# Optimization experiments

Measured on AMD Instinct MI355X. Metric: run time of the kernel, lower is better.

Reference implementation:

```python
import jax, jax.numpy as jnp
import numpy as np

NEG_SLOPE = 0.01  # torch nn.LeakyReLU default
N_NODES, N_EDGES, N_BATCH, L_PATH = 100000, 300000, 50000, 4
D_EMB, D_HID, N_HEADS = 128, 64, 8


def setup_inputs() -> dict:
    key = jax.random.key(0)
    ks = jax.random.split(key, 10)
    return {
        "batch_nodes": jax.random.randint(ks[0], (N_BATCH,), 0, N_NODES),
        "metapath_indices": jax.random.randint(ks[1], (N_EDGES, L_PATH), 0, N_NODES),
        "edge_dst": jax.random.randint(ks[2], (N_EDGES,), 0, N_NODES),
        "transformed_feature": jax.random.normal(ks[3], (N_NODES, D_EMB), jnp.float32),
        "W_i": jax.random.normal(ks[4], (D_HID, D_EMB), jnp.float32) * 0.05,
        "W_p": jax.random.normal(ks[5], (D_HID, D_EMB), jnp.float32) * 0.05,
        "attn": jax.random.normal(ks[6], (1, N_HEADS, D_HID), jnp.float32) * 0.05,
        "W_th": jax.random.normal(ks[7], (N_HEADS, N_HEADS), jnp.float32) * 0.3,
        "W_gate": jax.random.normal(ks[8], (1, D_HID), jnp.float32) * 0.1,
        "b_gate": jnp.zeros((1,), jnp.float32),
    }


def reference(batch_nodes, metapath_indices, edge_dst, transformed_feature,
              W_i, W_p, attn, W_th, W_gate, b_gate):
    N = transformed_feature.shape[0]
    # node_type_specific_agg for mtype==1: h_src/h_dst through linear_i, h_p1/h_p2 through linear_p
    membd = transformed_feature[metapath_indices]                      # [E, 4, D_emb]
    edata = (membd[:, 0] + membd[:, 3]) @ W_i.T \
          + (membd[:, 1] + membd[:, 2]) @ W_p.T                        # [E, D]
    E, D = edata.shape
    H = attn.shape[1]
    # cat([edata]*H, dim=1).view(-1, H, D) duplicates edata per head
    efeat = jnp.broadcast_to(edata[:, None, :], (E, H, D))             # [E, H, D]
    # talking-heads attention logits, leaky-relu
    logits = (efeat * attn).sum(-1) @ W_th.T                           # [E, H]
    logits = jax.nn.leaky_relu(logits, NEG_SLOPE)
    # dgl edge_softmax: per-dst-node, per-head softmax over incoming edges (stable)
    m = jax.ops.segment_max(logits, edge_dst, num_segments=N)          # [N, H]
    ex = jnp.exp(logits - m[edge_dst])                                 # [E, H]
    den = jax.ops.segment_sum(ex, edge_dst, num_segments=N)            # [N, H]
    a = ex / den[edge_dst]                                             # [E, H]  (dropout rate 0)
    # message passing: ft = efeature * a, summed per dst node
    msgs = (efeat * a[:, :, None]).reshape(E, H * D)
    node_ft = jax.ops.segment_sum(msgs, edge_dst, num_segments=N)      # [N, H*D]
    result = node_ft[batch_nodes].reshape(-1, H, D)                    # [B, H, D]
    # gated multi-head attention: gate = mean over batch of fc_gate(result)
    gate = jnp.mean(result @ W_gate.T + b_gate, axis=0)                # [H, 1]
    result = result * gate[None]                                       # [B, H, D]
    return result.reshape(-1, H * D)
```

## Files before the change

### kernel.cpp

```cpp
#include <hip/hip_runtime.h>
#include <cstdint>
#include <cstddef>


typedef __attribute__((ext_vector_type(8))) short bf16x8;
typedef __attribute__((ext_vector_type(4))) float f32x4;

__device__ __forceinline__ unsigned short f2bf(float f) {
    unsigned u = __float_as_uint(f);
    unsigned r = u + 0x7fffu + ((u >> 16) & 1u);
    return (unsigned short)(r >> 16);
}
__device__ __forceinline__ float bf2f(unsigned short h) {
    return __uint_as_float((unsigned)h << 16);
}

__global__ __launch_bounds__(256) void k_prep(
    const float* __restrict__ Wi, const float* __restrict__ Wp,
    unsigned short* __restrict__ Whi, unsigned short* __restrict__ Wlo,
    const int* __restrict__ batch_nodes, int* __restrict__ mult, int B) {
    int t = blockIdx.x * 256 + threadIdx.x;
    if (t < B) atomicAdd(&mult[batch_nodes[t]], 1);
    if (t >= 16384) return;
    int j = t & 7, L = (t >> 3) & 63, c = (t >> 9) & 7, s = t >> 12;
    int k = s * 32 + (L >> 4) * 8 + j;
    int n = c * 16 + (L & 15);
    float v = (n < 64) ? Wi[n * 128 + k] : Wp[(n - 64) * 128 + k];
    unsigned short h = f2bf(v);
    Whi[t] = h;
    Wlo[t] = f2bf(v - bf2f(h));
}

__global__ __launch_bounds__(256) void k_dense(
    const float* __restrict__ feat, const unsigned short* __restrict__ Whi,
    const unsigned short* __restrict__ Wlo, const float* __restrict__ attn,
    unsigned short* __restrict__ Ybf, float* __restrict__ P, int M) {
    __shared__ unsigned short sBh[4096];
    __shared__ unsigned short sBl[4096];
    int t = threadIdx.x;
    int wave = t >> 6;
    int L = t & 63;
    int m = L & 15, q = L >> 4;
    int R0 = blockIdx.x * 64 + wave * 16;

    f32x4 acc[8];
#pragma unroll
    for (int c = 0; c < 8; ++c) acc[c] = (f32x4){0.f, 0.f, 0.f, 0.f};

    int rowc = R0 + m; if (rowc > M - 1) rowc = M - 1;
    const float* arow = feat + (size_t)rowc * 128;

    for (int s = 0; s < 4; ++s) {
        __syncthreads();
        {
            bf16x8* shp = (bf16x8*)sBh;
            bf16x8* slp = (bf16x8*)sBl;
            const bf16x8* gh = (const bf16x8*)(Whi + s * 4096);
            const bf16x8* gl = (const bf16x8*)(Wlo + s * 4096);
            shp[t] = gh[t]; shp[t + 256] = gh[t + 256];
            slp[t] = gl[t]; slp[t + 256] = gl[t + 256];
        }
        __syncthreads();

        const float4* ap = (const float4*)(arow + s * 32 + q * 8);
        float4 a0 = ap[0], a1 = ap[1];
        float av[8] = {a0.x, a0.y, a0.z, a0.w, a1.x, a1.y, a1.z, a1.w};
        bf16x8 ahi, alo;
#pragma unroll
        for (int j = 0; j < 8; ++j) {
            unsigned short h = f2bf(av[j]);
            ahi[j] = (short)h;
            alo[j] = (short)f2bf(av[j] - bf2f(h));
        }
#pragma unroll
        for (int c = 0; c < 8; ++c) {
            const bf16x8 bh = *(const bf16x8*)(sBh + c * 512 + L * 8);
            const bf16x8 bl = *(const bf16x8*)(sBl + c * 512 + L * 8);
            acc[c] = __builtin_amdgcn_mfma_f32_16x16x32_bf16(ahi, bh, acc[c], 0, 0, 0);
            acc[c] = __builtin_amdgcn_mfma_f32_16x16x32_bf16(ahi, bl, acc[c], 0, 0, 0);
            acc[c] = __builtin_amdgcn_mfma_f32_16x16x32_bf16(alo, bh, acc[c], 0, 0, 0);
        }
    }
#pragma unroll
    for (int c = 0; c < 8; ++c) {
#pragma unroll
        for (int r = 0; r < 4; ++r) {
            int row = R0 + q * 4 + r;
            if (row < M) Ybf[(size_t)row * 128 + c * 16 + m] = f2bf(acc[c][r]);
        }
    }
#pragma unroll
    for (int i = 0; i < 8; ++i) {
        float a0 = attn[i * 64 + m];
        float a1 = attn[i * 64 + 16 + m];
        float a2 = attn[i * 64 + 32 + m];
        float a3 = attn[i * 64 + 48 + m];
#pragma unroll
        for (int r = 0; r < 4; ++r) {
            int row = R0 + q * 4 + r;
            float pi = acc[0][r] * a0 + acc[1][r] * a1 + acc[2][r] * a2 + acc[3][r] * a3;
            float pp = acc[4][r] * a0 + acc[5][r] * a1 + acc[6][r] * a2 + acc[7][r] * a3;
#pragma unroll
            for (int o = 1; o < 16; o <<= 1) {
                pi += __shfl_xor(pi, o);
                pp += __shfl_xor(pp, o);
            }
            if (row < M) {
                if (m == i)     P[(size_t)row * 16 + i] = pi;
                if (m == i + 8) P[(size_t)row * 16 + 8 + i] = pp;
            }
        }
    }
}

__global__ __launch_bounds__(256) void k_hist(
    const int* __restrict__ edge_dst, const int* __restrict__ mult,
    int* __restrict__ count, int E) {
    int e = blockIdx.x * 256 + threadIdx.x;
    if (e >= E) return;
    int d = edge_dst[e];
    if (mult[d] > 0) atomicAdd(&count[d], 1);
}

__global__ __launch_bounds__(256) void k_scan1(
    const int* __restrict__ count, int* __restrict__ excl, int* __restrict__ partials, int N) {
    __shared__ int lds[256];
    int t = threadIdx.x, i = blockIdx.x * 256 + t;
    int c = (i < N) ? count[i] : 0;
    lds[t] = c; __syncthreads();
    for (int o = 1; o < 256; o <<= 1) {
        int v = (t >= o) ? lds[t - o] : 0;
        __syncthreads(); lds[t] += v; __syncthreads();
    }
    if (i < N) excl[i] = lds[t] - c;
    if (t == 255) partials[blockIdx.x] = lds[255];
}

__global__ __launch_bounds__(256) void k_scan23(
    const int* __restrict__ excl, const int* __restrict__ partials,
    int* __restrict__ offsets, int* __restrict__ cursor, int N) {
    __shared__ int sacc[256];
    int bid = blockIdx.x, t = threadIdx.x;
    int s = 0;
    for (int j = t; j < bid; j += 256) s += partials[j];
    sacc[t] = s; __syncthreads();
#pragma unroll
    for (int o = 128; o > 0; o >>= 1) {
        if (t < o) sacc[t] += sacc[t + o];
        __syncthreads();
    }
    int boff = sacc[0];
    int i = bid * 256 + t;
    if (i < N) {
        int o = excl[i] + boff;
        offsets[i] = o; cursor[i] = o;
    }
    if (t == 0 && bid == gridDim.x - 1) offsets[N] = boff + partials[bid];
}

__global__ __launch_bounds__(256) void k_scatter_logits(
    const int* __restrict__ edge_dst, const int* __restrict__ mult,
    int* __restrict__ cursor, const int* __restrict__ mp,
    const float* __restrict__ P, const float* __restrict__ Wth,
    float* __restrict__ logits, int4* __restrict__ mpc, int E) {
    int e = blockIdx.x * 32 + (threadIdx.x >> 3);
    if (e >= E) return;
    int h = threadIdx.x & 7;
    int d = edge_dst[e];
    if (mult[d] == 0) return;
    int pos = 0;
    if (h == 0) pos = atomicAdd(&cursor[d], 1);
    int gbase = threadIdx.x & ~7;
    pos = __shfl(pos, gbase);
    int4 rows = *(const int4*)(mp + (size_t)e * 4);
    float s = P[(size_t)rows.x * 16 + h] + P[(size_t)rows.w * 16 + h]
            + P[(size_t)rows.y * 16 + 8 + h] + P[(size_t)rows.z * 16 + 8 + h];
    float l = 0.f;
#pragma unroll
    for (int j = 0; j < 8; ++j) {
        float sj = __shfl(s, gbase + j);
        l += Wth[h * 8 + j] * sj;
    }
    l = l > 0.f ? l : 0.01f * l;
    logits[(size_t)pos * 8 + h] = l;
    if (h == 0) mpc[pos] = rows;
}

__global__ __launch_bounds__(256) void k_node_agg(
    const unsigned short* __restrict__ Ybf, const float* __restrict__ logits,
    const int4* __restrict__ mpc, const int* __restrict__ offsets,
    const int* __restrict__ mult, const float* __restrict__ Wg,
    unsigned short* __restrict__ nftb, float* __restrict__ gate_part, int N) {
    int n = blockIdx.x * 4 + (threadIdx.x >> 6);
    int lane = threadIdx.x & 63;
    if (n >= N) return;
    int m = mult[n];
    if (m == 0) return;
    int beg = offsets[n], end = offsets[n + 1];

    float mx[8], den[8], acc[8];
#pragma unroll
    for (int h = 0; h < 8; ++h) { mx[h] = -1e30f; den[h] = 0.f; acc[h] = 0.f; }

    for (int j = beg; j < end; ++j) {
        const float4* lp = (const float4*)(logits + (size_t)j * 8);
        float4 l0 = lp[0], l1 = lp[1];
        int4 rows = mpc[j];
        float ed = bf2f(Ybf[(size_t)rows.x * 128 + lane])
                 + bf2f(Ybf[(size_t)rows.w * 128 + lane])
                 + bf2f(Ybf[(size_t)rows.y * 128 + 64 + lane])
                 + bf2f(Ybf[(size_t)rows.z * 128 + 64 + lane]);
#define OSM_STEP(H, LV)                                            \
        {                                                          \
            float nm = fmaxf(mx[H], (LV));                         \
            float cr = __expf(mx[H] - nm);                         \
            float w  = __expf((LV) - nm);                          \
            den[H] = den[H] * cr + w;                              \
            acc[H] = acc[H] * cr + w * ed;                         \
            mx[H] = nm;                                            \
        }
        OSM_STEP(0, l0.x) OSM_STEP(1, l0.y) OSM_STEP(2, l0.z) OSM_STEP(3, l0.w)
        OSM_STEP(4, l1.x) OSM_STEP(5, l1.y) OSM_STEP(6, l1.z) OSM_STEP(7, l1.w)
#undef OSM_STEP
    }
#pragma unroll
    for (int h = 0; h < 8; ++h) {
        float r = (end > beg) ? 1.f / den[h] : 0.f;
        acc[h] *= r;
    }

    unsigned short* base = nftb + (size_t)n * 512;
#pragma unroll
    for (int h = 0; h < 8; ++h) base[h * 64 + lane] = f2bf(acc[h]);

    float wg = Wg[lane];
    float myg = 0.f;
#pragma unroll
    for (int h = 0; h < 8; ++h) {
        float p = acc[h] * wg;
#pragma unroll
        for (int o = 32; o > 0; o >>= 1) p += __shfl_xor(p, o);
        if (lane == h) myg = p;
    }
    if (lane < 8)
        atomicAdd(&gate_part[(blockIdx.x & 1023) * 8 + lane], (float)m * myg);
}

__global__ __launch_bounds__(256) void k_gatefinal(
    const float* __restrict__ gate_part, const float* __restrict__ b_gate,
    float* __restrict__ gate, int B) {
    __shared__ float lds[256];
    int t = threadIdx.x;
    int h = t & 7, g = t >> 3;
    float s = 0.f;
    for (int b = g; b < 1024; b += 32) s += gate_part[b * 8 + h];
    lds[t] = s; __syncthreads();
    if (t < 8) {
        float tot = 0.f;
        for (int gg = 0; gg < 32; ++gg) tot += lds[gg * 8 + t];
        gate[t] = tot / (float)B + b_gate[0];
    }
}

__global__ __launch_bounds__(256) void k_output(
    const unsigned short* __restrict__ nftb, const int* __restrict__ batch_nodes,
    const float* __restrict__ gate, float* __restrict__ out, int B) {
    int idx = blockIdx.x * 256 + threadIdx.x;
    int total = B * 128;
    if (idx >= total) return;
    int b = idx >> 7;
    int rem4 = idx & 127;
    int h = rem4 >> 4;
    int n = batch_nodes[b];
    ushort4 v = *(const ushort4*)(nftb + (size_t)n * 512 + rem4 * 4);
    float g = gate[h];
    float4 o;
    o.x = bf2f(v.x) * g; o.y = bf2f(v.y) * g;
    o.z = bf2f(v.z) * g; o.w = bf2f(v.w) * g;
    *(float4*)(out + (size_t)idx * 4) = o;
}

extern "C" void kernel_launch(void* const* d_in, const int* in_sizes, int n_in,
                              void* d_out, int out_size, void* d_ws, size_t ws_size,
                              hipStream_t stream) {
    const int*   batch_nodes = (const int*)d_in[0];
    const int*   mp          = (const int*)d_in[1];
    const int*   edge_dst    = (const int*)d_in[2];
    const float* feat        = (const float*)d_in[3];
    const float* W_i         = (const float*)d_in[4];
    const float* W_p         = (const float*)d_in[5];
    const float* attn        = (const float*)d_in[6];
    const float* W_th        = (const float*)d_in[7];
    const float* W_gate      = (const float*)d_in[8];
    const float* b_gate      = (const float*)d_in[9];
    float* out = (float*)d_out;

    const int B = in_sizes[0];
    const int E = in_sizes[2];
    const int N = in_sizes[3] / 128;
    const int nb_scan = (N + 255) / 256;

    char* w = (char*)d_ws;
    auto alloc = [&](size_t bytes) -> void* {
        void* p = (void*)w;
        w += (bytes + 255) & ~(size_t)255;
        return p;
    };
    unsigned short* Whi = (unsigned short*)alloc(16384 * 2);
    unsigned short* Wlo = (unsigned short*)alloc(16384 * 2);
    unsigned short* Ybf = (unsigned short*)alloc((size_t)N * 128 * 2);
    float* P            = (float*)alloc((size_t)N * 16 * 4);
    float* logits       = (float*)alloc((size_t)E * 8 * 4);
    int4*  mpc          = (int4*)alloc((size_t)E * 16);
    size_t zero_bytes   = (size_t)N * 4 + (size_t)N * 4 + 1024 * 8 * 4;
    int*   mult         = (int*)alloc(zero_bytes);
    int*   count        = mult + N;
    float* gate_part    = (float*)(count + N);
    int*   excl         = (int*)alloc((size_t)N * 4);
    int*   offsets      = (int*)alloc((size_t)(N + 1) * 4);
    int*   cursor       = (int*)alloc((size_t)N * 4);
    int*   partials     = (int*)alloc(512 * 4);
    unsigned short* nftb = (unsigned short*)alloc((size_t)N * 512 * 2);
    float* gate         = (float*)alloc(256);

    hipMemsetAsync(mult, 0, zero_bytes, stream);

    int prep_work = (B > 16384) ? B : 16384;
    k_prep<<<(prep_work + 255) / 256, 256, 0, stream>>>(W_i, W_p, Whi, Wlo,
                                                        batch_nodes, mult, B);
    k_dense<<<(N + 63) / 64, 256, 0, stream>>>(feat, Whi, Wlo, attn, Ybf, P, N);

    k_hist<<<(E + 255) / 256, 256, 0, stream>>>(edge_dst, mult, count, E);
    k_scan1<<<nb_scan, 256, 0, stream>>>(count, excl, partials, N);
    k_scan23<<<nb_scan, 256, 0, stream>>>(excl, partials, offsets, cursor, N);
    k_scatter_logits<<<(E + 31) / 32, 256, 0, stream>>>(edge_dst, mult, cursor,
                                                        mp, P, W_th, logits, mpc, E);
    k_node_agg<<<(N + 3) / 4, 256, 0, stream>>>(Ybf, logits, mpc, offsets, mult,
                                                W_gate, nftb, gate_part, N);
    k_gatefinal<<<1, 256, 0, stream>>>(gate_part, b_gate, gate, B);
    k_output<<<(B * 128 + 255) / 256, 256, 0, stream>>>(nftb, batch_nodes, gate, out, B);
}
```

Measured before the change: 317.5 us.

## Fuse all stages into one persistent kernel with software grid barriers

Replaces the nine separate kernel launches with a single persistent cooperative-style kernel sized to device occupancy, separating phases with an atomic generation-counter grid barrier. It also overlaps the edge histogram with the dense GEMM phase and folds the gate finalization into per-block shared memory. This removes launch gaps and tail effects between small kernels, but relies on all blocks being co-resident (no cooperative launch guarantee) and caps parallelism per phase at the persistent grid size.

Measured after the change: 933.5 us. 2.94x slower.

```diff
diff --git a/kernel.cpp b/kernel.cpp
--- a/kernel.cpp
+++ b/kernel.cpp
@@ -15,269 +15,298 @@
     return __uint_as_float((unsigned)h << 16);
 }
 
-__global__ __launch_bounds__(256) void k_prep(
+__device__ __forceinline__ void gsync(unsigned* cnt, unsigned* gen, unsigned nb) {
+    __syncthreads();
+    if (threadIdx.x == 0) {
+        unsigned g = __hip_atomic_load(gen, __ATOMIC_RELAXED, __HIP_MEMORY_SCOPE_AGENT);
+        unsigned arrived = __hip_atomic_fetch_add(cnt, 1u, __ATOMIC_ACQ_REL,
+                                                  __HIP_MEMORY_SCOPE_AGENT);
+        if (arrived == nb - 1u) {
+            __hip_atomic_store(cnt, 0u, __ATOMIC_RELAXED, __HIP_MEMORY_SCOPE_AGENT);
+            __hip_atomic_store(gen, g + 1u, __ATOMIC_RELEASE, __HIP_MEMORY_SCOPE_AGENT);
+        } else {
+            while (__hip_atomic_load(gen, __ATOMIC_ACQUIRE,
+                                     __HIP_MEMORY_SCOPE_AGENT) == g)
+                __builtin_amdgcn_s_sleep(1);
+        }
+    }
+    __syncthreads();
+}
+
+__global__ __launch_bounds__(256, 4) void k_mega(
+    const int* __restrict__ batch_nodes, const int* __restrict__ mp,
+    const int* __restrict__ edge_dst, const float* __restrict__ feat,
     const float* __restrict__ Wi, const float* __restrict__ Wp,
+    const float* __restrict__ attn, const float* __restrict__ Wth,
+    const float* __restrict__ Wg, const float* __restrict__ bg,
+    float* __restrict__ out,
     unsigned short* __restrict__ Whi, unsigned short* __restrict__ Wlo,
-    const int* __restrict__ batch_nodes, int* __restrict__ mult, int B) {
-    int t = blockIdx.x * 256 + threadIdx.x;
-    if (t < B) atomicAdd(&mult[batch_nodes[t]], 1);
-    if (t >= 16384) return;
-    int j = t & 7, L = (t >> 3) & 63, c = (t >> 9) & 7, s = t >> 12;
-    int k = s * 32 + (L >> 4) * 8 + j;
-    int n = c * 16 + (L & 15);
-    float v = (n < 64) ? Wi[n * 128 + k] : Wp[(n - 64) * 128 + k];
-    unsigned short h = f2bf(v);
-    Whi[t] = h;
-    Wlo[t] = f2bf(v - bf2f(h));
-}
-
-__global__ __launch_bounds__(256) void k_dense(
-    const float* __restrict__ feat, const unsigned short* __restrict__ Whi,
-    const unsigned short* __restrict__ Wlo, const float* __restrict__ attn,
-    unsigned short* __restrict__ Ybf, float* __restrict__ P, int M) {
-    __shared__ unsigned short sBh[4096];
-    __shared__ unsigned short sBl[4096];
-    int t = threadIdx.x;
-    int wave = t >> 6;
-    int L = t & 63;
-    int m = L & 15, q = L >> 4;
-    int R0 = blockIdx.x * 64 + wave * 16;
-
-    f32x4 acc[8];
-#pragma unroll
-    for (int c = 0; c < 8; ++c) acc[c] = (f32x4){0.f, 0.f, 0.f, 0.f};
-
-    int rowc = R0 + m; if (rowc > M - 1) rowc = M - 1;
-    const float* arow = feat + (size_t)rowc * 128;
-
-    for (int s = 0; s < 4; ++s) {
+    unsigned short* __restrict__ Ybf, float* __restrict__ P,
+    float* __restrict__ logits, int4* __restrict__ mpc,
+    int* __restrict__ mult, int* __restrict__ count,
+    float* __restrict__ gate_part, int* __restrict__ offsets,
+    int* __restrict__ cursor, int* __restrict__ partials,
+    unsigned short* __restrict__ nftb, unsigned* __restrict__ bar,
+    int N, int E, int B, int nb) {
+
+    __shared__ union {
+        struct { unsigned short h[4096]; unsigned short l[4096]; } stage;
+        int   scan[256];
+        float fred[256];
+    } sm;
+    __shared__ float sgate[8];
+
+    const int bid = blockIdx.x, tid = threadIdx.x;
+    const int gtid = bid * 256 + tid;
+    const int nthreads = nb * 256;
+    unsigned* cnt = bar;
+    unsigned* gen = bar + 1;
+
+    for (int t = gtid; t < 16384; t += nthreads) {
+        int j = t & 7, L = (t >> 3) & 63, c = (t >> 9) & 7, s = t >> 12;
+        int k = s * 32 + (L >> 4) * 8 + j;
+        int n = c * 16 + (L & 15);
+        float v = (n < 64) ? Wi[n * 128 + k] : Wp[(n - 64) * 128 + k];
+        unsigned short h = f2bf(v);
+        Whi[t] = h;
+        Wlo[t] = f2bf(v - bf2f(h));
+    }
+    for (int i = gtid; i < B; i += nthreads)
+        atomicAdd(&mult[batch_nodes[i]], 1);
+    gsync(cnt, gen, nb);
+
+    for (int e = gtid; e < E; e += nthreads) {
+        int d = edge_dst[e];
+        if (mult[d] > 0) atomicAdd(&count[d], 1);
+    }
+    {
+        const int wave = tid >> 6;
+        const int L = tid & 63;
+        const int m = L & 15, q = L >> 4;
+        const int ntiles = (N + 63) >> 6;
+        for (int tile = bid; tile < ntiles; tile += nb) {
+            int R0 = tile * 64 + wave * 16;
+            f32x4 acc[8];
+#pragma unroll
+            for (int c = 0; c < 8; ++c) acc[c] = (f32x4){0.f, 0.f, 0.f, 0.f};
+            int rowc = R0 + m; if (rowc > N - 1) rowc = N - 1;
+            const float* arow = feat + (size_t)rowc * 128;
+
+            for (int s = 0; s < 4; ++s) {
+                __syncthreads();
+                {
+                    bf16x8* shp = (bf16x8*)sm.stage.h;
+                    bf16x8* slp = (bf16x8*)sm.stage.l;
+                    const bf16x8* gh = (const bf16x8*)(Whi + s * 4096);
+                    const bf16x8* gl = (const bf16x8*)(Wlo + s * 4096);
+                    shp[tid] = gh[tid]; shp[tid + 256] = gh[tid + 256];
+                    slp[tid] = gl[tid]; slp[tid + 256] = gl[tid + 256];
+                }
+                __syncthreads();
+
+                const float4* ap = (const float4*)(arow + s * 32 + q * 8);
+                float4 a0 = ap[0], a1 = ap[1];
+                float av[8] = {a0.x, a0.y, a0.z, a0.w, a1.x, a1.y, a1.z, a1.w};
+                bf16x8 ahi, alo;
+#pragma unroll
+                for (int j = 0; j < 8; ++j) {
+                    unsigned short h = f2bf(av[j]);
+                    ahi[j] = (short)h;
+                    alo[j] = (short)f2bf(av[j] - bf2f(h));
+                }
+#pragma unroll
+                for (int c = 0; c < 8; ++c) {
+                    const bf16x8 bh = *(const bf16x8*)(sm.stage.h + c * 512 + L * 8);
+                    const bf16x8 bl = *(const bf16x8*)(sm.stage.l + c * 512 + L * 8);
+                    acc[c] = __builtin_amdgcn_mfma_f32_16x16x32_bf16(ahi, bh, acc[c], 0, 0, 0);
+                    acc[c] = __builtin_amdgcn_mfma_f32_16x16x32_bf16(ahi, bl, acc[c], 0, 0, 0);
+                    acc[c] = __builtin_amdgcn_mfma_f32_16x16x32_bf16(alo, bh, acc[c], 0, 0, 0);
+                }
+            }
+#pragma unroll
+            for (int c = 0; c < 8; ++c) {
+#pragma unroll
+                for (int r = 0; r < 4; ++r) {
+                    int row = R0 + q * 4 + r;
+                    if (row < N) Ybf[(size_t)row * 128 + c * 16 + m] = f2bf(acc[c][r]);
+                }
+            }
+#pragma unroll
+            for (int i = 0; i < 8; ++i) {
+                float a0 = attn[i * 64 + m];
+                float a1 = attn[i * 64 + 16 + m];
+                float a2 = attn[i * 64 + 32 + m];
+                float a3 = attn[i * 64 + 48 + m];
+#pragma unroll
+                for (int r = 0; r < 4; ++r) {
+                    int row = R0 + q * 4 + r;
+                    float pi = acc[0][r] * a0 + acc[1][r] * a1 + acc[2][r] * a2 + acc[3][r] * a3;
+                    float pp = acc[4][r] * a0 + acc[5][r] * a1 + acc[6][r] * a2 + acc[7][r] * a3;
+#pragma unroll
+                    for (int o = 1; o < 16; o <<= 1) {
+                        pi += __shfl_xor(pi, o);
+                        pp += __shfl_xor(pp, o);
+                    }
+                    if (row < N) {
+                        if (m == i)     P[(size_t)row * 16 + i] = pi;
+                        if (m == i + 8) P[(size_t)row * 16 + 8 + i] = pp;
+                    }
+                }
+            }
+        }
+    }
+    gsync(cnt, gen, nb);
+
+    const int nchunks = (N + 255) >> 8;
+    for (int chunk = bid; chunk < nchunks; chunk += nb) {
+        int i = chunk * 256 + tid;
+        int c = (i < N) ? count[i] : 0;
+        sm.scan[tid] = c; __syncthreads();
+#pragma unroll
+        for (int o = 128; o > 0; o >>= 1) {
+            if (tid < o) sm.scan[tid] += sm.scan[tid + o];
+            __syncthreads();
+        }
+        if (tid == 0) partials[chunk] = sm.scan[0];
         __syncthreads();
-        {
-            bf16x8* shp = (bf16x8*)sBh;
-            bf16x8* slp = (bf16x8*)sBl;
-            const bf16x8* gh = (const bf16x8*)(Whi + s * 4096);
-            const bf16x8* gl = (const bf16x8*)(Wlo + s * 4096);
-            shp[t] = gh[t]; shp[t + 256] = gh[t + 256];
-            slp[t] = gl[t]; slp[t + 256] = gl[t + 256];
-        }
+    }
+    gsync(cnt, gen, nb);
+
+    for (int chunk = bid; chunk < nchunks; chunk += nb) {
+        int s = 0;
+        for (int j = tid; j < chunk; j += 256) s += partials[j];
+        sm.scan[tid] = s; __syncthreads();
+#pragma unroll
+        for (int o = 128; o > 0; o >>= 1) {
+            if (tid < o) sm.scan[tid] += sm.scan[tid + o];
+            __syncthreads();
+        }
+        int boff = sm.scan[0]; __syncthreads();
+        int i = chunk * 256 + tid;
+        int c = (i < N) ? count[i] : 0;
+        sm.scan[tid] = c; __syncthreads();
+        for (int o = 1; o < 256; o <<= 1) {
+            int v = (tid >= o) ? sm.scan[tid - o] : 0;
+            __syncthreads(); sm.scan[tid] += v; __syncthreads();
+        }
+        int off = boff + sm.scan[tid] - c;
+        if (i < N) { offsets[i] = off; cursor[i] = off; }
+        if (tid == 255 && chunk == nchunks - 1) offsets[N] = boff + sm.scan[255];
         __syncthreads();
-
-        const float4* ap = (const float4*)(arow + s * 32 + q * 8);
-        float4 a0 = ap[0], a1 = ap[1];
-        float av[8] = {a0.x, a0.y, a0.z, a0.w, a1.x, a1.y, a1.z, a1.w};
-        bf16x8 ahi, alo;
-#pragma unroll
-        for (int j = 0; j < 8; ++j) {
-            unsigned short h = f2bf(av[j]);
-            ahi[j] = (short)h;
-            alo[j] = (short)f2bf(av[j] - bf2f(h));
-        }
-#pragma unroll
-        for (int c = 0; c < 8; ++c) {
-            const bf16x8 bh = *(const bf16x8*)(sBh + c * 512 + L * 8);
-            const bf16x8 bl = *(const bf16x8*)(sBl + c * 512 + L * 8);
-            acc[c] = __builtin_amdgcn_mfma_f32_16x16x32_bf16(ahi, bh, acc[c], 0, 0, 0);
-            acc[c] = __builtin_amdgcn_mfma_f32_16x16x32_bf16(ahi, bl, acc[c], 0, 0, 0);
-            acc[c] = __builtin_amdgcn_mfma_f32_16x16x32_bf16(alo, bh, acc[c], 0, 0, 0);
-        }
-    }
-#pragma unroll
-    for (int c = 0; c < 8; ++c) {
-#pragma unroll
-        for (int r = 0; r < 4; ++r) {
-            int row = R0 + q * 4 + r;
-            if (row < M) Ybf[(size_t)row * 128 + c * 16 + m] = f2bf(acc[c][r]);
-        }
-    }
-#pragma unroll
-    for (int i = 0; i < 8; ++i) {
-        float a0 = attn[i * 64 + m];
-        float a1 = attn[i * 64 + 16 + m];
-        float a2 = attn[i * 64 + 32 + m];
-        float a3 = attn[i * 64 + 48 + m];
-#pragma unroll
-        for (int r = 0; r < 4; ++r) {
-            int row = R0 + q * 4 + r;
-            float pi = acc[0][r] * a0 + acc[1][r] * a1 + acc[2][r] * a2 + acc[3][r] * a3;
-            float pp = acc[4][r] * a0 + acc[5][r] * a1 + acc[6][r] * a2 + acc[7][r] * a3;
-#pragma unroll
-            for (int o = 1; o < 16; o <<= 1) {
-                pi += __shfl_xor(pi, o);
-                pp += __shfl_xor(pp, o);
-            }
-            if (row < M) {
-                if (m == i)     P[(size_t)row * 16 + i] = pi;
-                if (m == i + 8) P[(size_t)row * 16 + 8 + i] = pp;
-            }
-        }
-    }
-}
-
-__global__ __launch_bounds__(256) void k_hist(
-    const int* __restrict__ edge_dst, const int* __restrict__ mult,
-    int* __restrict__ count, int E) {
-    int e = blockIdx.x * 256 + threadIdx.x;
-    if (e >= E) return;
-    int d = edge_dst[e];
-    if (mult[d] > 0) atomicAdd(&count[d], 1);
-}
-
-__global__ __launch_bounds__(256) void k_scan1(
-    const int* __restrict__ count, int* __restrict__ excl, int* __restrict__ partials, int N) {
-    __shared__ int lds[256];
-    int t = threadIdx.x, i = blockIdx.x * 256 + t;
-    int c = (i < N) ? count[i] : 0;
-    lds[t] = c; __syncthreads();
-    for (int o = 1; o < 256; o <<= 1) {
-        int v = (t >= o) ? lds[t - o] : 0;
-        __syncthreads(); lds[t] += v; __syncthreads();
-    }
-    if (i < N) excl[i] = lds[t] - c;
-    if (t == 255) partials[blockIdx.x] = lds[255];
-}
-
-__global__ __launch_bounds__(256) void k_scan23(
-    const int* __restrict__ excl, const int* __restrict__ partials,
-    int* __restrict__ offsets, int* __restrict__ cursor, int N) {
-    __shared__ int sacc[256];
-    int bid = blockIdx.x, t = threadIdx.x;
-    int s = 0;
-    for (int j = t; j < bid; j += 256) s += partials[j];
-    sacc[t] = s; __syncthreads();
-#pragma unroll
-    for (int o = 128; o > 0; o >>= 1) {
-        if (t < o) sacc[t] += sacc[t + o];
+    }
+    gsync(cnt, gen, nb);
+
+    {
+        int grp = tid >> 3;
+        int h = tid & 7;
+        int gbase = tid & ~7;
+        for (int e = bid * 32 + grp; e < E; e += nb * 32) {
+            int d = edge_dst[e];
+            if (mult[d] == 0) continue;
+            int pos = 0;
+            if (h == 0) pos = atomicAdd(&cursor[d], 1);
+            pos = __shfl(pos, gbase);
+            int4 rows = *(const int4*)(mp + (size_t)e * 4);
+            float s = P[(size_t)rows.x * 16 + h] + P[(size_t)rows.w * 16 + h]
+                    + P[(size_t)rows.y * 16 + 8 + h] + P[(size_t)rows.z * 16 + 8 + h];
+            float l = 0.f;
+#pragma unroll
+            for (int j = 0; j < 8; ++j) {
+                float sj = __shfl(s, gbase + j);
+                l += Wth[h * 8 + j] * sj;
+            }
+            l = l > 0.f ? l : 0.01f * l;
+            logits[(size_t)pos * 8 + h] = l;
+            if (h == 0) mpc[pos] = rows;
+        }
+    }
+    gsync(cnt, gen, nb);
+
+    {
+        int lane = tid & 63;
+        int gwave = bid * 4 + (tid >> 6);
+        float wg = Wg[lane];
+        for (int n = gwave; n < N; n += nb * 4) {
+            int mlt = mult[n];
+            if (mlt == 0) continue;
+            int beg = offsets[n], end = offsets[n + 1];
+
+            float mx[8], den[8], acc[8];
+#pragma unroll
+            for (int h = 0; h < 8; ++h) { mx[h] = -1e30f; den[h] = 0.f; acc[h] = 0.f; }
+
+            for (int j = beg; j < end; ++j) {
+                const float4* lp = (const float4*)(logits + (size_t)j * 8);
+                float4 l0 = lp[0], l1 = lp[1];
+                int4 rows = mpc[j];
+                float ed = bf2f(Ybf[(size_t)rows.x * 128 + lane])
+                         + bf2f(Ybf[(size_t)rows.w * 128 + lane])
+                         + bf2f(Ybf[(size_t)rows.y * 128 + 64 + lane])
+                         + bf2f(Ybf[(size_t)rows.z * 128 + 64 + lane]);
+#define OSM_STEP(H, LV)                                            \
+                {                                                  \
+                    float nm = fmaxf(mx[H], (LV));                 \
+                    float cr = __expf(mx[H] - nm);                 \
+                    float w  = __expf((LV) - nm);                  \
+                    den[H] = den[H] * cr + w;                      \
+                    acc[H] = acc[H] * cr + w * ed;                 \
+                    mx[H] = nm;                                    \
+                }
+                OSM_STEP(0, l0.x) OSM_STEP(1, l0.y) OSM_STEP(2, l0.z) OSM_STEP(3, l0.w)
+                OSM_STEP(4, l1.x) OSM_STEP(5, l1.y) OSM_STEP(6, l1.z) OSM_STEP(7, l1.w)
+#undef OSM_STEP
+            }
+#pragma unroll
+            for (int h = 0; h < 8; ++h) {
+                float r = (end > beg) ? 1.f / den[h] : 0.f;
+                acc[h] *= r;
+            }
+
+            unsigned short* base = nftb + (size_t)n * 512;
+#pragma unroll
+            for (int h = 0; h < 8; ++h) base[h * 64 + lane] = f2bf(acc[h]);
+
+            float myg = 0.f;
+#pragma unroll
+            for (int h = 0; h < 8; ++h) {
+                float p = acc[h] * wg;
+#pragma unroll
+                for (int o = 32; o > 0; o >>= 1) p += __shfl_xor(p, o);
+                if (lane == h) myg = p;
+            }
+            if (lane < 8)
+                atomicAdd(&gate_part[bid * 8 + lane], (float)mlt * myg);
+        }
+    }
+    gsync(cnt, gen, nb);
+
+    {
+        int hh = tid & 7, g = tid >> 3;
+        float s = 0.f;
+        for (int b = g; b < 1024; b += 32) s += gate_part[b * 8 + hh];
+        sm.fred[tid] = s; __syncthreads();
+        if (tid < 8) {
+            float tot = 0.f;
+            for (int gg = 0; gg < 32; ++gg) tot += sm.fred[gg * 8 + tid];
+            sgate[tid] = tot / (float)B + bg[0];
+        }
         __syncthreads();
     }
-    int boff = sacc[0];
-    int i = bid * 256 + t;
-    if (i < N) {
-        int o = excl[i] + boff;
-        offsets[i] = o; cursor[i] = o;
-    }
-    if (t == 0 && bid == gridDim.x - 1) offsets[N] = boff + partials[bid];
-}
-
-__global__ __launch_bounds__(256) void k_scatter_logits(
-    const int* __restrict__ edge_dst, const int* __restrict__ mult,
-    int* __restrict__ cursor, const int* __restrict__ mp,
-    const float* __restrict__ P, const float* __restrict__ Wth,
-    float* __restrict__ logits, int4* __restrict__ mpc, int E) {
-    int e = blockIdx.x * 32 + (threadIdx.x >> 3);
-    if (e >= E) return;
-    int h = threadIdx.x & 7;
-    int d = edge_dst[e];
-    if (mult[d] == 0) return;
-    int pos = 0;
-    if (h == 0) pos = atomicAdd(&cursor[d], 1);
-    int gbase = threadIdx.x & ~7;
-    pos = __shfl(pos, gbase);
-    int4 rows = *(const int4*)(mp + (size_t)e * 4);
-    float s = P[(size_t)rows.x * 16 + h] + P[(size_t)rows.w * 16 + h]
-            + P[(size_t)rows.y * 16 + 8 + h] + P[(size_t)rows.z * 16 + 8 + h];
-    float l = 0.f;
-#pragma unroll
-    for (int j = 0; j < 8; ++j) {
-        float sj = __shfl(s, gbase + j);
-        l += Wth[h * 8 + j] * sj;
-    }
-    l = l > 0.f ? l : 0.01f * l;
-    logits[(size_t)pos * 8 + h] = l;
-    if (h == 0) mpc[pos] = rows;
-}
-
-__global__ __launch_bounds__(256) void k_node_agg(
-    const unsigned short* __restrict__ Ybf, const float* __restrict__ logits,
-    const int4* __restrict__ mpc, const int* __restrict__ offsets,
-    const int* __restrict__ mult, const float* __restrict__ Wg,
-    unsigned short* __restrict__ nftb, float* __restrict__ gate_part, int N) {
-    int n = blockIdx.x * 4 + (threadIdx.x >> 6);
-    int lane = threadIdx.x & 63;
-    if (n >= N) return;
-    int m = mult[n];
-    if (m == 0) return;
-    int beg = offsets[n], end = offsets[n + 1];
-
-    float mx[8], den[8], acc[8];
-#pragma unroll
-    for (int h = 0; h < 8; ++h) { mx[h] = -1e30f; den[h] = 0.f; acc[h] = 0.f; }
-
-    for (int j = beg; j < end; ++j) {
-        const float4* lp = (const float4*)(logits + (size_t)j * 8);
-        float4 l0 = lp[0], l1 = lp[1];
-        int4 rows = mpc[j];
-        float ed = bf2f(Ybf[(size_t)rows.x * 128 + lane])
-                 + bf2f(Ybf[(size_t)rows.w * 128 + lane])
-                 + bf2f(Ybf[(size_t)rows.y * 128 + 64 + lane])
-                 + bf2f(Ybf[(size_t)rows.z * 128 + 64 + lane]);
-#define OSM_STEP(H, LV)                                            \
-        {                                                          \
-            float nm = fmaxf(mx[H], (LV));                         \
-            float cr = __expf(mx[H] - nm);                         \
-            float w  = __expf((LV) - nm);                          \
-            den[H] = den[H] * cr + w;                              \
-            acc[H] = acc[H] * cr + w * ed;                         \
-            mx[H] = nm;                                            \
-        }
-        OSM_STEP(0, l0.x) OSM_STEP(1, l0.y) OSM_STEP(2, l0.z) OSM_STEP(3, l0.w)
-        OSM_STEP(4, l1.x) OSM_STEP(5, l1.y) OSM_STEP(6, l1.z) OSM_STEP(7, l1.w)
-#undef OSM_STEP
-    }
-#pragma unroll
-    for (int h = 0; h < 8; ++h) {
-        float r = (end > beg) ? 1.f / den[h] : 0.f;
-        acc[h] *= r;
-    }
-
-    unsigned short* base = nftb + (size_t)n * 512;
-#pragma unroll
-    for (int h = 0; h < 8; ++h) base[h * 64 + lane] = f2bf(acc[h]);
-
-    float wg = Wg[lane];
-    float myg = 0.f;
-#pragma unroll
-    for (int h = 0; h < 8; ++h) {
-        float p = acc[h] * wg;
-#pragma unroll
-        for (int o = 32; o > 0; o >>= 1) p += __shfl_xor(p, o);
-        if (lane == h) myg = p;
-    }
-    if (lane < 8)
-        atomicAdd(&gate_part[(blockIdx.x & 1023) * 8 + lane], (float)m * myg);
-}
-
-__global__ __launch_bounds__(256) void k_gatefinal(
-    const float* __restrict__ gate_part, const float* __restrict__ b_gate,
-    float* __restrict__ gate, int B) {
-    __shared__ float lds[256];
-    int t = threadIdx.x;
-    int h = t & 7, g = t >> 3;
-    float s = 0.f;
-    for (int b = g; b < 1024; b += 32) s += gate_part[b * 8 + h];
-    lds[t] = s; __syncthreads();
-    if (t < 8) {
-        float tot = 0.f;
-        for (int gg = 0; gg < 32; ++gg) tot += lds[gg * 8 + t];
-        gate[t] = tot / (float)B + b_gate[0];
-    }
-}
-
-__global__ __launch_bounds__(256) void k_output(
-    const unsigned short* __restrict__ nftb, const int* __restrict__ batch_nodes,
-    const float* __restrict__ gate, float* __restrict__ out, int B) {
-    int idx = blockIdx.x * 256 + threadIdx.x;
-    int total = B * 128;
-    if (idx >= total) return;
-    int b = idx >> 7;
-    int rem4 = idx & 127;
-    int h = rem4 >> 4;
-    int n = batch_nodes[b];
-    ushort4 v = *(const ushort4*)(nftb + (size_t)n * 512 + rem4 * 4);
-    float g = gate[h];
-    float4 o;
-    o.x = bf2f(v.x) * g; o.y = bf2f(v.y) * g;
-    o.z = bf2f(v.z) * g; o.w = bf2f(v.w) * g;
-    *(float4*)(out + (size_t)idx * 4) = o;
+    {
+        int total = B * 128;
+        for (int idx = gtid; idx < total; idx += nthreads) {
+            int b = idx >> 7;
+            int rem = idx & 127;
+            int hh = rem >> 4;
+            int n = batch_nodes[b];
+            ushort4 v = *(const ushort4*)(nftb + (size_t)n * 512 + rem * 4);
+            float g = sgate[hh];
+            float4 o;
+            o.x = bf2f(v.x) * g; o.y = bf2f(v.y) * g;
+            o.z = bf2f(v.z) * g; o.w = bf2f(v.w) * g;
+            *(float4*)(out + (size_t)idx * 4) = o;
+        }
+    }
 }
 
 extern "C" void kernel_launch(void* const* d_in, const int* in_sizes, int n_in,
@@ -298,7 +327,6 @@
     const int B = in_sizes[0];
     const int E = in_sizes[2];
     const int N = in_sizes[3] / 128;
-    const int nb_scan = (N + 255) / 256;
 
     char* w = (char*)d_ws;
     auto alloc = [&](size_t bytes) -> void* {
@@ -312,31 +340,37 @@
     float* P            = (float*)alloc((size_t)N * 16 * 4);
     float* logits       = (float*)alloc((size_t)E * 8 * 4);
     int4*  mpc          = (int4*)alloc((size_t)E * 16);
-    size_t zero_bytes   = (size_t)N * 4 + (size_t)N * 4 + 1024 * 8 * 4;
-    int*   mult         = (int*)alloc(zero_bytes);
+    size_t zero_ints    = (size_t)2 * N + 8192 + 16;
+    int*   mult         = (int*)alloc(zero_ints * 4);
     int*   count        = mult + N;
     float* gate_part    = (float*)(count + N);
-    int*   excl         = (int*)alloc((size_t)N * 4);
+    unsigned* bar       = (unsigned*)(gate_part + 8192);
     int*   offsets      = (int*)alloc((size_t)(N + 1) * 4);
     int*   cursor       = (int*)alloc((size_t)N * 4);
     int*   partials     = (int*)alloc(512 * 4);
     unsigned short* nftb = (unsigned short*)alloc((size_t)N * 512 * 2);
-    float* gate         = (float*)alloc(256);
-
-    hipMemsetAsync(mult, 0, zero_bytes, stream);
-
-    int prep_work = (B > 16384) ? B : 16384;
-    k_prep<<<(prep_work + 255) / 256, 256, 0, stream>>>(W_i, W_p, Whi, Wlo,
-                                                        batch_nodes, mult, B);
-    k_dense<<<(N + 63) / 64, 256, 0, stream>>>(feat, Whi, Wlo, attn, Ybf, P, N);
-
-    k_hist<<<(E + 255) / 256, 256, 0, stream>>>(edge_dst, mult, count, E);
-    k_scan1<<<nb_scan, 256, 0, stream>>>(count, excl, partials, N);
-    k_scan23<<<nb_scan, 256, 0, stream>>>(excl, partials, offsets, cursor, N);
-    k_scatter_logits<<<(E + 31) / 32, 256, 0, stream>>>(edge_dst, mult, cursor,
-                                                        mp, P, W_th, logits, mpc, E);
-    k_node_agg<<<(N + 3) / 4, 256, 0, stream>>>(Ybf, logits, mpc, offsets, mult,
-                                                W_gate, nftb, gate_part, N);
-    k_gatefinal<<<1, 256, 0, stream>>>(gate_part, b_gate, gate, B);
-    k_output<<<(B * 128 + 255) / 256, 256, 0, stream>>>(nftb, batch_nodes, gate, out, B);
-}
+
+    static int nb_cached = 0;
+    if (nb_cached == 0) {
+        int occ = 0;
+        hipError_t err = hipOccupancyMaxActiveBlocksPerMultiprocessor(
+            &occ, reinterpret_cast<const void*>(k_mega), 256, 0);
+        if (err != hipSuccess || occ < 1) occ = 1;
+        hipDeviceProp_t prop;
+        int mpc_count = 256;
+        if (hipGetDeviceProperties(&prop, 0) == hipSuccess)
+            mpc_count = prop.multiProcessorCount;
+        long nb = (long)occ * mpc_count;
+        if (nb > 1024) nb = 1024;
+        if (nb < 1) nb = 1;
+        nb_cached = (int)nb;
+    }
+    const int nb = nb_cached;
+
+    hipMemsetAsync(mult, 0, zero_ints * 4, stream);
+    k_mega<<<nb, 256, 0, stream>>>(batch_nodes, mp, edge_dst, feat, W_i, W_p,
+                                   attn, W_th, W_gate, b_gate, out,
+                                   Whi, Wlo, Ybf, P, logits, mpc,
+                                   mult, count, gate_part, offsets, cursor,
+                                   partials, nftb, bar, N, E, B, nb);
+}
```
